# Performance work log

Hardware: AMD Instinct MI355X
Metric: run time of the kernel (lower is better)

## Reference

```python
import jax, jax.numpy as jnp
import numpy as np

B, S, D, H = 64, 1024, 256, 256


def setup_inputs() -> dict:
    key = jax.random.key(0)
    k1, k2, k3, k4, k5 = jax.random.split(key, 5)
    stdv = 1.0 / np.sqrt(H)
    x = jax.random.normal(k1, (B, S, D), dtype=jnp.float32)
    modality_lambda = jax.random.uniform(k2, (S,), dtype=jnp.float32)
    W = jax.random.uniform(k3, (D, 4 * H), minval=-stdv, maxval=stdv, dtype=jnp.float32)
    U = jax.random.uniform(k4, (H, 4 * H), minval=-stdv, maxval=stdv, dtype=jnp.float32)
    bias = jax.random.uniform(k5, (4 * H,), minval=-stdv, maxval=stdv, dtype=jnp.float32)
    return {"x": x, "modality_lambda": modality_lambda, "W": W, "U": U, "bias": bias}


def reference(x, modality_lambda, W, U, bias):
    hs = U.shape[0]
    bs = x.shape[0]
    # Precompute input projection for all timesteps in one GEMM: [S, B, 4H]
    x_proj = jnp.einsum('bsd,dg->sbg', x, W) + bias
    h0 = jnp.zeros((bs, hs), x.dtype)
    c0 = jnp.zeros((bs, hs), x.dtype)

    def step(carry, inp):
        h, c = carry
        xp, lam = inp
        gates = xp + h @ U  # [B, 4H]
        i_t = jax.nn.sigmoid(gates[:, :hs])
        f_t = jax.nn.sigmoid(gates[:, hs:2 * hs])
        g_t = jnp.tanh(gates[:, 2 * hs:3 * hs])
        o_t = jax.nn.sigmoid(gates[:, 3 * hs:])
        c = f_t * c + i_t * g_t * lam
        h = o_t * jnp.tanh(c)
        return (h, c), h

    (h_t, c_t), hidden_seq = jax.lax.scan(step, (h0, c0), (x_proj, modality_lambda))
    hidden_seq = jnp.transpose(hidden_seq, (1, 0, 2))  # [B, S, H]
    return hidden_seq, h_t, c_t
```

## Files before the change

### kernel.cpp

```cpp
#include <hip/hip_runtime.h>
#include <hip/hip_bf16.h>


#define BSH 16777216u
#define BH  16384u

typedef short short8 __attribute__((ext_vector_type(8)));
typedef float float4_ __attribute__((ext_vector_type(4)));
typedef unsigned int uint2_ __attribute__((ext_vector_type(2)));
typedef unsigned int uint4_ __attribute__((ext_vector_type(4)));

static __device__ __forceinline__ unsigned short f2bf(float f) {
    unsigned int u = __builtin_bit_cast(unsigned int, f);
    u += 0x7FFFu + ((u >> 16) & 1u);
    return (unsigned short)(u >> 16);
}
static __device__ __forceinline__ float bf2f(unsigned short h) {
    unsigned int u = ((unsigned int)h) << 16;
    return __builtin_bit_cast(float, u);
}
static __device__ __forceinline__ uint4_ pack8(const unsigned short* t) {
    uint4_ v;
    v.x = (unsigned int)t[0] | ((unsigned int)t[1] << 16);
    v.y = (unsigned int)t[2] | ((unsigned int)t[3] << 16);
    v.z = (unsigned int)t[4] | ((unsigned int)t[5] << 16);
    v.w = (unsigned int)t[6] | ((unsigned int)t[7] << 16);
    return v;
}
static __device__ __forceinline__ unsigned umin_(unsigned a, unsigned b) {
    return a < b ? a : b;
}
static __device__ __forceinline__ unsigned pkmin16(unsigned a, unsigned b) {
    unsigned d;
    asm("v_pk_min_u16 %0, %1, %2" : "=v"(d) : "v"(a), "v"(b));
    return d;
}
static __device__ __forceinline__ void gload_lds16(const void* g, void* l) {
    __builtin_amdgcn_global_load_lds(
        (const __attribute__((address_space(1))) unsigned int*)g,
        (__attribute__((address_space(3))) unsigned int*)l, 16, 0, 0);
}
static __device__ __forceinline__ void barrier_lgkm() {
    asm volatile("s_waitcnt lgkmcnt(0)" ::: "memory");
    __builtin_amdgcn_s_barrier();
    asm volatile("" ::: "memory");
}

__global__ void prep_kernel(const float* __restrict__ W, const float* __restrict__ U,
                            const float* __restrict__ bias,
                            unsigned short* __restrict__ Wbf, unsigned short* __restrict__ Ubf,
                            float* __restrict__ biasf) {
    int tid = blockIdx.x * blockDim.x + threadIdx.x;
    if (tid < 65536) {
        int idx = tid & 32767;
        const bool isU = (tid >= 32768);
        const float* src = isU ? U : W;
        unsigned short* dst = isU ? Ubf : Wbf;
        int sl = idx >> 9, kt = (idx >> 6) & 7, lane = idx & 63;
        int c = lane & 15, kgrp = lane >> 4;
        int m = sl >> 3, wv = sl & 7;
        int gatec = c >> 2, jj = c & 3;
        int ncol = gatec * 256 + 32 * m + 4 * wv + jj;
        unsigned short t8[8];
#pragma unroll
        for (int e = 0; e < 8; e++) {
            int k = kt * 32 + kgrp * 8 + e;
            float v = src[k * 1024 + ncol];
            t8[e] = f2bf(isU ? -v : v);
        }
        *(uint4_*)(dst + (size_t)idx * 8) = pack8(t8);
    } else if (tid < 66560) {
        int idx2 = tid - 65536;
        int sl = idx2 >> 4, c = idx2 & 15;
        int m = sl >> 3, wv = sl & 7, gatec = c >> 2, jj = c & 3;
        int ncol = gatec * 256 + 32 * m + 4 * wv + jj;
        biasf[idx2] = bias[ncol];
    }
}

__global__ __launch_bounds__(512, 2)
void xproj_kernel(const float* __restrict__ x, const unsigned short* __restrict__ Wbf,
                  const float* __restrict__ biasf, unsigned short* __restrict__ xp) {
    const int bx = blockIdx.x;
    const int g = bx & 3, tile = bx >> 2;
    const int s0 = tile * 4;
    const int tidx = threadIdx.x;
    const int w = tidx >> 6, lane = tidx & 63;

    __shared__ unsigned short Afrag[4][8][64][8];

    {
        int row = tidx >> 3;
        int kt = tidx & 7;
        int si = row >> 4, r = row & 15;
        int b = g * 16 + r, s = s0 + si;
        const float* px = x + ((size_t)b * 1024 + s) * 256 + kt * 32;
#pragma unroll
        for (int kg = 0; kg < 4; kg++) {
            float4_ v0 = *(const float4_*)(px + kg * 8);
            float4_ v1 = *(const float4_*)(px + kg * 8 + 4);
            unsigned short t8[8] = { f2bf(v0.x), f2bf(v0.y), f2bf(v0.z), f2bf(v0.w),
                                     f2bf(v1.x), f2bf(v1.y), f2bf(v1.z), f2bf(v1.w) };
            *(uint4_*)&Afrag[si][kt][kg * 16 + r][0] = pack8(t8);
        }
    }
    __syncthreads();

    float4_ acc[8][4];
#pragma unroll
    for (int q = 0; q < 8; q++) {
        int sl = w * 8 + q;
        float bv = biasf[sl * 16 + (lane & 15)];
#pragma unroll
        for (int si = 0; si < 4; si++) acc[q][si] = (float4_){bv, bv, bv, bv};
    }
#pragma unroll
    for (int kt = 0; kt < 8; kt++) {
        short8 a[4];
#pragma unroll
        for (int si = 0; si < 4; si++)
            a[si] = *(const short8*)&Afrag[si][kt][lane][0];
#pragma unroll
        for (int q = 0; q < 8; q++) {
            short8 bfr = *(const short8*)(Wbf + (((size_t)(w * 8 + q) * 8 + kt) * 64 + lane) * 8);
#pragma unroll
            for (int si = 0; si < 4; si++)
                acc[q][si] = __builtin_amdgcn_mfma_f32_16x16x32_bf16(a[si], bfr, acc[q][si], 0, 0, 0);
        }
    }
#pragma unroll
    for (int q = 0; q < 8; q++) {
        int sl = w * 8 + q;
        int wgx = g * 8 + (sl >> 3);
#pragma unroll
        for (int si = 0; si < 4; si++) {
            int s = s0 + si;
            unsigned int lo = (unsigned int)f2bf(acc[q][si].x) | ((unsigned int)f2bf(acc[q][si].y) << 16);
            unsigned int hi = (unsigned int)f2bf(acc[q][si].z) | ((unsigned int)f2bf(acc[q][si].w) << 16);
            uint2_ v = {lo, hi};
            *(uint2_*)(xp + ((((size_t)wgx * 1024 + s) * 8 + (sl & 7)) * 64 + lane) * 4) = v;
        }
    }
}

__global__ __launch_bounds__(640, 1)
void lstm_kernel(const unsigned short* __restrict__ Ubf,
                 const unsigned short* __restrict__ xp,
                 const float* __restrict__ lam,
                 unsigned short* __restrict__ hslow,
                 unsigned short* __restrict__ hfast,
                 float* __restrict__ out) {
    const int bx = blockIdx.x;
    const int g = bx & 7;
    if (g >= 4) return;
    const int m = bx >> 3;
    const int tid = threadIdx.x;
    const int w = tid >> 6, lane = tid & 63;

    __shared__ float lamLDS[1024];
    __shared__ alignas(16) unsigned short htmp[2][16][40];
    __shared__ alignas(16) unsigned short xpring[8][2048];
    __shared__ alignas(16) unsigned short hstage[2][8][64][8];

    ((unsigned int*)htmp)[tid] = 0u;
    for (int i = tid; i < 1024; i += 640) lamLDS[i] = lam[i];

    const int col = lane & 15;
    const int gatec = col >> 2, jj = col & 3;
    const int rr0 = (lane >> 4) * 4;
    const bool active = (gatec == 0);
    const bool fast_en = (hfast != nullptr);

    short8 u[8];
    if (w < 8) {
        int sl = m * 8 + w;
#pragma unroll
        for (int kt = 0; kt < 8; kt++)
            u[kt] = *(const short8*)(Ubf + (((size_t)sl * 8 + kt) * 64 + lane) * 8);
    }

    const size_t wgx = (size_t)(g * 8 + m);

    if (w < 8 && fast_en) {
        char* pz = (char*)hfast + ((size_t)g << 13) + (size_t)w * 1024 + (size_t)lane * 16;
        uint4_ z = {0u, 0u, 0u, 0u};
        for (int tt = 0; tt < 1024; tt++) {
            asm volatile("global_store_dwordx4 %0, %1, off sc0" :: "v"(pz), "v"(z) : "memory");
            pz += 32768;
        }
    }

    if (w == 8) {
        for (int s = 0; s < 6; s++) {
            const char* src = (const char*)xp + ((wgx * 1024 + s) << 12) + (size_t)lane * 16;
            char* dst = (char*)&xpring[s][0];
#pragma unroll
            for (int c2 = 0; c2 < 4; c2++)
                gload_lds16(src + c2 * 1024, dst + c2 * 1024);
        }
        asm volatile("s_waitcnt vmcnt(20)" ::: "memory");
    }

    float cst[4] = {0.f, 0.f, 0.f, 0.f};
    barrier_lgkm();

    const int u_col = 4 * w + jj;
    char* hpubF = (char*)hfast + ((size_t)g << 13) + (size_t)m * 1024
                + (size_t)((u_col >> 3) * 256 + rr0 * 16 + (u_col & 7) * 2);
    const char* pf = (const char*)hfast + ((size_t)g << 13) + (size_t)w * 1024
                   + (size_t)lane * 16 - 32768;
    const char* pb = (const char*)hslow + ((size_t)g << 13) + (size_t)w * 1024
                   + (size_t)lane * 16 - 32768;
    char* hps = (char*)hslow + ((size_t)g << 13) + (size_t)m * 1024 + (size_t)lane * 16;

    bool use_fast = fast_en;

    for (int t = 0; t < 1024; t++) {
        if (w < 8) {
            if (t > 0) {
                uint4_ r;
                bool got = false;
                if (use_fast) {
                    for (int k = 0; k < 12; k++) {
                        asm volatile("global_load_dwordx4 %0, %1, off sc0\n\t"
                                     "s_waitcnt vmcnt(0)"
                                     : "=v"(r) : "v"(pf) : "memory");
                        __builtin_amdgcn_sched_barrier(0);
                        unsigned mm = pkmin16(pkmin16(r.x, r.y), pkmin16(r.z, r.w));
                        if (__all(((mm & 0xffffu) != 0u) && ((mm >> 16) != 0u))) {
                            got = true; break;
                        }
                    }
                    if (!got && t > 8) use_fast = false;
                }
                if (!got) {
                    for (;;) {
                        asm volatile("global_load_dwordx4 %0, %1, off sc0 sc1\n\t"
                                     "s_waitcnt vmcnt(0)"
                                     : "=v"(r) : "v"(pb) : "memory");
                        __builtin_amdgcn_sched_barrier(0);
                        if (__all(umin_(umin_(r.x, r.y), umin_(r.z, r.w)) != 0u)) break;
                    }
                }
                *(uint4_*)&hstage[t & 1][w][lane][0] = r;
            }
        } else if (w == 8) {
            if (t + 6 < 1024) {
                int slot = (t + 6) & 7;
                const char* src = (const char*)xp + ((wgx * 1024 + (size_t)(t + 6)) << 12)
                                  + (size_t)lane * 16;
                char* dst = (char*)&xpring[slot][0];
#pragma unroll
                for (int c2 = 0; c2 < 4; c2++)
                    gload_lds16(src + c2 * 1024, dst + c2 * 1024);
            }
            if (t == 0)            asm volatile("s_waitcnt vmcnt(20)" ::: "memory");
            else if (t == 1)       asm volatile("s_waitcnt vmcnt(22)" ::: "memory");
            else if (t + 6 < 1024) asm volatile("s_waitcnt vmcnt(24)" ::: "memory");
            else                   asm volatile("s_waitcnt vmcnt(0)"  ::: "memory");
        }
        barrier_lgkm();
        if (w < 8) {
            unsigned long long xpd =
                *(const unsigned long long*)&xpring[t & 7][w * 256 + lane * 4];
            float4_ acc0, acc1 = (float4_){0.f, 0.f, 0.f, 0.f};
            acc0.x = bf2f((unsigned short)(xpd & 0xffff));
            acc0.y = bf2f((unsigned short)((xpd >> 16) & 0xffff));
            acc0.z = bf2f((unsigned short)((xpd >> 32) & 0xffff));
            acc0.w = bf2f((unsigned short)(xpd >> 48));

            if (t > 0) {
                short8 a0 = *(const short8*)&hstage[t & 1][0][lane][0];
                short8 a1 = *(const short8*)&hstage[t & 1][1][lane][0];
                short8 a2 = *(const short8*)&hstage[t & 1][2][lane][0];
                short8 a3 = *(const short8*)&hstage[t & 1][3][lane][0];
                short8 a4 = *(const short8*)&hstage[t & 1][4][lane][0];
                short8 a5 = *(const short8*)&hstage[t & 1][5][lane][0];
                short8 a6 = *(const short8*)&hstage[t & 1][6][lane][0];
                short8 a7 = *(const short8*)&hstage[t & 1][7][lane][0];
                acc0 = __builtin_amdgcn_mfma_f32_16x16x32_bf16(a0, u[0], acc0, 0, 0, 0);
                acc1 = __builtin_amdgcn_mfma_f32_16x16x32_bf16(a1, u[1], acc1, 0, 0, 0);
                acc0 = __builtin_amdgcn_mfma_f32_16x16x32_bf16(a2, u[2], acc0, 0, 0, 0);
                acc1 = __builtin_amdgcn_mfma_f32_16x16x32_bf16(a3, u[3], acc1, 0, 0, 0);
                acc0 = __builtin_amdgcn_mfma_f32_16x16x32_bf16(a4, u[4], acc0, 0, 0, 0);
                acc1 = __builtin_amdgcn_mfma_f32_16x16x32_bf16(a5, u[5], acc1, 0, 0, 0);
                acc0 = __builtin_amdgcn_mfma_f32_16x16x32_bf16(a6, u[6], acc0, 0, 0, 0);
                acc1 = __builtin_amdgcn_mfma_f32_16x16x32_bf16(a7, u[7], acc1, 0, 0, 0);
            }

            float lamt = lamLDS[t];
            float gv[4], fv[4], ggv[4], ov[4];
#pragma unroll
            for (int q = 0; q < 4; q++) {
                float xg = acc0[q] + acc1[q];
                float y = (gatec == 2) ? 2.f * xg : xg;
                float sgm = 1.f / (1.f + __expf(-y));
                gv[q] = (gatec == 2) ? 2.f * sgm - 1.f : sgm;
            }
#pragma unroll
            for (int q = 0; q < 4; q++) {
                fv[q]  = __shfl(gv[q], lane + 4, 64);
                ggv[q] = __shfl(gv[q], lane + 8, 64);
                ov[q]  = __shfl(gv[q], lane + 12, 64);
            }
            if (active) {
                float hq[4];
                unsigned short hb[4];
#pragma unroll
                for (int q = 0; q < 4; q++) {
                    float c = fv[q] * cst[q] + gv[q] * ggv[q] * lamt;
                    cst[q] = c;
                    float th = 2.f / (1.f + __expf(-2.f * c)) - 1.f;
                    hq[q] = ov[q] * th;
                    unsigned short b = f2bf(-hq[q]);
                    if (b == 0) b = 0x8000u;
                    hb[q] = b;
                }
                if (fast_en) {
                    asm volatile("global_store_short %0, %1, off sc0"           :: "v"(hpubF), "v"((unsigned)hb[0]) : "memory");
                    asm volatile("global_store_short %0, %1, off offset:16 sc0" :: "v"(hpubF), "v"((unsigned)hb[1]) : "memory");
                    asm volatile("global_store_short %0, %1, off offset:32 sc0" :: "v"(hpubF), "v"((unsigned)hb[2]) : "memory");
                    asm volatile("global_store_short %0, %1, off offset:48 sc0" :: "v"(hpubF), "v"((unsigned)hb[3]) : "memory");
                }
#pragma unroll
                for (int q = 0; q < 4; q++)
                    htmp[t & 1][rr0 + q][4 * w + jj] = hb[q];
                if (t == 1023) {
#pragma unroll
                    for (int q = 0; q < 4; q++) {
                        size_t b = (size_t)g * 16 + rr0 + q;
                        int j = m * 32 + 4 * w + jj;
                        out[BSH + b * 256 + j] = hq[q];
                        out[BSH + BH + b * 256 + j] = cst[q];
                    }
                }
            }
        } else if (w == 9) {
            int r_ = lane & 15, kg = lane >> 4;
            volatile unsigned int* hp32 =
                (volatile unsigned int*)&htmp[t & 1][r_][kg * 8];
            unsigned a0, a1, a2, a3;
            for (;;) {
                a0 = hp32[0]; a1 = hp32[1]; a2 = hp32[2]; a3 = hp32[3];
                unsigned mm = pkmin16(pkmin16(a0, a1), pkmin16(a2, a3));
                if (__all(((mm & 0xffffu) != 0u) && ((mm >> 16) != 0u))) break;
            }
            uint4_ blk = {a0, a1, a2, a3};
            asm volatile("global_store_dwordx4 %0, %1, off sc0 sc1"
                         :: "v"(hps), "v"(blk) : "memory");
            unsigned x0 = a0 ^ 0x80008000u, x1 = a1 ^ 0x80008000u;
            unsigned x2 = a2 ^ 0x80008000u, x3 = a3 ^ 0x80008000u;
            float4_ v0 = { bf2f((unsigned short)(x0 & 0xffff)), bf2f((unsigned short)(x0 >> 16)),
                           bf2f((unsigned short)(x1 & 0xffff)), bf2f((unsigned short)(x1 >> 16)) };
            float4_ v1 = { bf2f((unsigned short)(x2 & 0xffff)), bf2f((unsigned short)(x2 >> 16)),
                           bf2f((unsigned short)(x3 & 0xffff)), bf2f((unsigned short)(x3 >> 16)) };
            float* po = out + (((size_t)(g * 16 + r_)) << 18) + ((size_t)t << 8)
                        + m * 32 + kg * 8;
            *(float4_*)po = v0;
            *(float4_*)(po + 4) = v1;
            uint4_ z = {0u, 0u, 0u, 0u};
            *(uint4_*)&htmp[t & 1][r_][kg * 8] = z;
        }
        pf += 32768;
        pb += 32768;
        hpubF += 32768;
        hps += 32768;
    }
}

__global__ void ws_too_small_kernel(float* out) {
    if (threadIdx.x == 0 && blockIdx.x == 0) out[0] = -777777.0f;
}

extern "C" void kernel_launch(void* const* d_in, const int* in_sizes, int n_in,
                              void* d_out, int out_size, void* d_ws, size_t ws_size,
                              hipStream_t stream) {
    const float* x    = (const float*)d_in[0];
    const float* lam  = (const float*)d_in[1];
    const float* W    = (const float*)d_in[2];
    const float* U    = (const float*)d_in[3];
    const float* bias = (const float*)d_in[4];
    float* out = (float*)d_out;

    const size_t NEED_BASE = (size_t)162 << 20;
    const size_t NEED_FAST = (size_t)194 << 20;
    if (ws_size < NEED_BASE) {
        ws_too_small_kernel<<<1, 64, 0, stream>>>(out);
        return;
    }
    const bool fast_en = (ws_size >= NEED_FAST);
    char* ws = (char*)d_ws;
    unsigned short* Ubf   = (unsigned short*)(ws + (256 << 10));
    unsigned short* Wbf   = (unsigned short*)(ws + (768 << 10));
    float*          biasf = (float*)(ws + (1280 << 10));
    unsigned short* hslow = (unsigned short*)(ws + ((size_t)2 << 20));
    unsigned short* xp    = (unsigned short*)(ws + ((size_t)66 << 20));
    unsigned short* hfast = fast_en ? (unsigned short*)(ws + ((size_t)34 << 20)) : nullptr;

    hipMemsetAsync(hslow, 0, (size_t)32 << 20, stream);
    if (fast_en)
        hipMemsetAsync(hfast, 0, (size_t)32 << 20, stream);
    prep_kernel<<<260, 256, 0, stream>>>(W, U, bias, Wbf, Ubf, biasf);
    xproj_kernel<<<1024, 512, 0, stream>>>(x, Wbf, biasf, xp);
    lstm_kernel<<<64, 640, 0, stream>>>(Ubf, xp, lam, hslow, hfast, out);
}
```

Baseline: 2.079 ms.

## Assign LSTM workgroup roles by hardware XCD ID with atomic tickets

The recurrent kernel now reads each workgroup's XCD from the hardware register and takes an atomic ticket, so the 8 blocks of each batch group are guaranteed to share one XCD instead of relying on round-robin blockIdx mapping. The grid grows to 1024 blocks so enough land on each of XCDs 0-3; extra blocks exit at once. It also drops the in-kernel zeroing of the fast h buffer, which a host memset already does, and adds a bail-out counter to the slow spin loop. The risks are extra block launch overhead and the assumption that all 32 needed blocks become co-resident.

```diff
diff --git a/kernel.cpp b/kernel.cpp
--- a/kernel.cpp
+++ b/kernel.cpp
@@ -149,18 +149,32 @@
                  const float* __restrict__ lam,
                  unsigned short* __restrict__ hslow,
                  unsigned short* __restrict__ hfast,
+                 unsigned int* __restrict__ ticket,
                  float* __restrict__ out) {
-    const int bx = blockIdx.x;
-    const int g = bx & 7;
-    if (g >= 4) return;
-    const int m = bx >> 3;
     const int tid = threadIdx.x;
     const int w = tid >> 6, lane = tid & 63;
 
+    __shared__ int roleLDS[2];
     __shared__ float lamLDS[1024];
     __shared__ alignas(16) unsigned short htmp[2][16][40];
     __shared__ alignas(16) unsigned short xpring[8][2048];
     __shared__ alignas(16) unsigned short hstage[2][8][64][8];
+
+    if (tid == 0) {
+        unsigned xcd;
+        asm volatile("s_getreg_b32 %0, hwreg(HW_REG_XCC_ID)" : "=s"(xcd));
+        xcd &= 7u;
+        unsigned tk = 0xFFu;
+        if (xcd < 4u)
+            tk = __hip_atomic_fetch_add(&ticket[xcd], 1u,
+                                        __ATOMIC_RELAXED, __HIP_MEMORY_SCOPE_AGENT);
+        roleLDS[0] = (int)xcd;
+        roleLDS[1] = (int)tk;
+    }
+    __syncthreads();
+    const int g = roleLDS[0];
+    const int m = roleLDS[1];
+    if (g >= 4 || m >= 8) return;
 
     ((unsigned int*)htmp)[tid] = 0u;
     for (int i = tid; i < 1024; i += 640) lamLDS[i] = lam[i];
@@ -180,15 +194,6 @@
     }
 
     const size_t wgx = (size_t)(g * 8 + m);
-
-    if (w < 8 && fast_en) {
-        char* pz = (char*)hfast + ((size_t)g << 13) + (size_t)w * 1024 + (size_t)lane * 16;
-        uint4_ z = {0u, 0u, 0u, 0u};
-        for (int tt = 0; tt < 1024; tt++) {
-            asm volatile("global_store_dwordx4 %0, %1, off sc0" :: "v"(pz), "v"(z) : "memory");
-            pz += 32768;
-        }
-    }
 
     if (w == 8) {
         for (int s = 0; s < 6; s++) {
@@ -234,12 +239,14 @@
                     if (!got && t > 8) use_fast = false;
                 }
                 if (!got) {
+                    unsigned bail = 0;
                     for (;;) {
                         asm volatile("global_load_dwordx4 %0, %1, off sc0 sc1\n\t"
                                      "s_waitcnt vmcnt(0)"
                                      : "=v"(r) : "v"(pb) : "memory");
                         __builtin_amdgcn_sched_barrier(0);
                         if (__all(umin_(umin_(r.x, r.y), umin_(r.z, r.w)) != 0u)) break;
+                        if (++bail > (1u << 22)) break;
                     }
                 }
                 *(uint4_*)&hstage[t & 1][w][lane][0] = r;
@@ -390,6 +397,7 @@
     }
     const bool fast_en = (ws_size >= NEED_FAST);
     char* ws = (char*)d_ws;
+    unsigned int*   ticket = (unsigned int*)ws;
     unsigned short* Ubf   = (unsigned short*)(ws + (256 << 10));
     unsigned short* Wbf   = (unsigned short*)(ws + (768 << 10));
     float*          biasf = (float*)(ws + (1280 << 10));
@@ -397,10 +405,11 @@
     unsigned short* xp    = (unsigned short*)(ws + ((size_t)66 << 20));
     unsigned short* hfast = fast_en ? (unsigned short*)(ws + ((size_t)34 << 20)) : nullptr;
 
+    hipMemsetAsync(ticket, 0, 64, stream);
     hipMemsetAsync(hslow, 0, (size_t)32 << 20, stream);
     if (fast_en)
         hipMemsetAsync(hfast, 0, (size_t)32 << 20, stream);
     prep_kernel<<<260, 256, 0, stream>>>(W, U, bias, Wbf, Ubf, biasf);
     xproj_kernel<<<1024, 512, 0, stream>>>(x, Wbf, biasf, xp);
-    lstm_kernel<<<64, 640, 0, stream>>>(Ubf, xp, lam, hslow, hfast, out);
-}
+    lstm_kernel<<<1024, 640, 0, stream>>>(Ubf, xp, lam, hslow, hfast, ticket, out);
+}
```

Result: no change. 2.042 ms (-1.8%).
